# Kernel optimization log

Hardware: AMD Instinct MI355X
Metric: run time of the kernel (lower is better)

## Reference

```python
import jax, jax.numpy as jnp
import numpy as np

B, S, D = 4, 2048, 1024
EXPAND = 2
D_INNER = EXPAND * D          # 2048
D_CONV = 4
N_EXPERTS = 8
TOP_K = 2
ROUTER_HIDDEN = 128


def setup_inputs() -> dict:
    key = jax.random.key(0)
    ks = jax.random.split(key, 8)
    s = lambda fan_in: 1.0 / np.sqrt(fan_in)
    hidden_states = jax.random.normal(ks[0], (B, S, D), dtype=jnp.float32)
    # stacked per-expert SimpleSSM params (torch Linear weight layout: [out, in])
    in_proj_w = jax.random.uniform(ks[1], (N_EXPERTS, 2 * D_INNER, D), minval=-s(D), maxval=s(D), dtype=jnp.float32)
    conv_w = jax.random.uniform(ks[2], (N_EXPERTS, D_INNER, 1, D_CONV), minval=-s(D_CONV), maxval=s(D_CONV), dtype=jnp.float32)
    conv_b = jax.random.uniform(ks[3], (N_EXPERTS, D_INNER), minval=-s(D_CONV), maxval=s(D_CONV), dtype=jnp.float32)
    out_proj_w = jax.random.uniform(ks[4], (N_EXPERTS, D, D_INNER), minval=-s(D_INNER), maxval=s(D_INNER), dtype=jnp.float32)
    # router: Linear(D,128,bias=False) -> SiLU -> Linear(128,E,bias=False)
    router_w1 = jax.random.uniform(ks[5], (ROUTER_HIDDEN, D), minval=-s(D), maxval=s(D), dtype=jnp.float32)
    router_w2 = jax.random.uniform(ks[6], (N_EXPERTS, ROUTER_HIDDEN), minval=-s(ROUTER_HIDDEN), maxval=s(ROUTER_HIDDEN), dtype=jnp.float32)
    return {
        "hidden_states": hidden_states,
        "in_proj_w": in_proj_w,
        "conv_w": conv_w,
        "conv_b": conv_b,
        "out_proj_w": out_proj_w,
        "router_w1": router_w1,
        "router_w2": router_w2,
    }


def _simple_ssm(h, in_w, cw, cb, out_w):
    # h: [B,S,D]; in_w: [2*Di, D]; cw: [Di,1,4]; cb: [Di]; out_w: [D, Di]
    zx = jnp.einsum('bsd,ed->bse', h, in_w)           # [B,S,2*Di]
    z, x = jnp.split(zx, 2, axis=-1)                   # each [B,S,Di]
    xc = jnp.transpose(x, (0, 2, 1))                   # [B,Di,S]
    # torch Conv1d(padding=3, k=4) then truncate to S == causal pad (3,0) valid conv
    xc = jax.lax.conv_general_dilated(
        xc, cw, window_strides=(1,), padding=((D_CONV - 1, 0),),
        feature_group_count=D_INNER,
        dimension_numbers=('NCH', 'OIH', 'NCH'))
    xc = xc + cb[None, :, None]
    x = jnp.transpose(xc, (0, 2, 1))                   # [B,S,Di]
    x = jax.nn.silu(x) * jax.nn.silu(z)
    return jnp.einsum('bse,de->bsd', x, out_w)         # [B,S,D]


def _forward(hidden_states, in_proj_w, conv_w, conv_b, out_proj_w, router_w1, router_w2):
    # --- routing ---
    rh = jax.nn.silu(jnp.einsum('bsd,hd->bsh', hidden_states, router_w1))
    logits = jnp.einsum('bsh,eh->bse', rh, router_w2)          # [B,S,E]
    probs = jax.nn.softmax(logits, axis=-1)
    rw, sel = jax.lax.top_k(probs, TOP_K)                      # [B,S,K]
    rw = rw / jnp.sum(rw, axis=-1, keepdims=True)
    # combined per-token per-expert weight: sum_k 1[sel==e] * rw_k -> [B,S,E]
    comb = jnp.sum(jax.nn.one_hot(sel, N_EXPERTS, dtype=rw.dtype) * rw[..., None], axis=2)
    # --- each expert processes the FULL sequence ---
    expert_outs = jax.vmap(_simple_ssm, in_axes=(None, 0, 0, 0, 0))(
        hidden_states, in_proj_w, conv_w, conv_b, out_proj_w)  # [E,B,S,D]
    return jnp.einsum('ebsd,bse->bsd', expert_outs, comb)


def reference(hidden_states, in_proj_w, conv_w, conv_b, out_proj_w, router_w1, router_w2):
    return _forward(hidden_states, in_proj_w, conv_w, conv_b, out_proj_w, router_w1, router_w2)
```

## Files before the change

kernel.cpp:

```cpp
#include <hip/hip_runtime.h>
#include <hip/hip_bf16.h>
#include <stdint.h>

#define SLEN   2048
#define DMODEL 1024
#define DINNER 2048
#define NEXPERT 8
#define NTOK   8192

typedef __bf16  b8   __attribute__((ext_vector_type(8)));
typedef float   f4   __attribute__((ext_vector_type(4)));
typedef unsigned short u16x8 __attribute__((ext_vector_type(8)));

#define GLOAD16(gp, lp) __builtin_amdgcn_global_load_lds( \
    (const __attribute__((address_space(1))) uint32_t*)(gp), \
    (__attribute__((address_space(3))) uint32_t*)(lp), 16, 0, 0)

__device__ __forceinline__ unsigned short f2b(float f) {
  __hip_bfloat16 h = __float2bfloat16(f);
  return __builtin_bit_cast(unsigned short, h);
}
__device__ __forceinline__ float b2f(unsigned short u) {
  uint32_t x = ((uint32_t)u) << 16;
  return __builtin_bit_cast(float, x);
}
__device__ __forceinline__ float silu_f(float v) { return v / (1.0f + __expf(-v)); }

__global__ __launch_bounds__(256) void cast_f32_bf16(const float* __restrict__ in,
                                                     unsigned short* __restrict__ out, int n4) {
  int i = blockIdx.x * 256 + threadIdx.x;
  int stride = gridDim.x * 256;
  for (; i < n4; i += stride) {
    float4 v = ((const float4*)in)[i];
    ushort4 o;
    o.x = f2b(v.x); o.y = f2b(v.y); o.z = f2b(v.z); o.w = f2b(v.w);
    ((ushort4*)out)[i] = o;
  }
}

__global__ __launch_bounds__(256) void transpose_w1(const float* __restrict__ in,
                                                    float* __restrict__ out) {
  int idx = blockIdx.x * 256 + threadIdx.x;
  int k = idx >> 7, hd = idx & 127;
  out[idx] = in[hd * 1024 + k];
}

__global__ __launch_bounds__(256) void router_kernel(const float* __restrict__ h,
                                                     const float* __restrict__ w1T,
                                                     const float* __restrict__ w2,
                                                     float* __restrict__ comb) {
  __shared__ float hs[8 * 1024];
  __shared__ float red[2 * 8 * 128];
  __shared__ float lg[8 * 8];
  int tid = threadIdx.x;
  int t0 = blockIdx.x * 8;

  const float4* src = (const float4*)(h + (size_t)t0 * 1024);
  float4* dst = (float4*)hs;
#pragma unroll
  for (int i = 0; i < 8; ++i) dst[tid + i * 256] = src[tid + i * 256];
  __syncthreads();

  int hd = tid & 127, half = tid >> 7;
  float acc[8] = {0.f,0.f,0.f,0.f,0.f,0.f,0.f,0.f};
  int kbeg = half * 512;
  for (int k = kbeg; k < kbeg + 512; ++k) {
    float w = w1T[k * 128 + hd];
#pragma unroll
    for (int tok = 0; tok < 8; ++tok) acc[tok] += w * hs[tok * 1024 + k];
  }
#pragma unroll
  for (int tok = 0; tok < 8; ++tok) red[(half * 8 + tok) * 128 + hd] = acc[tok];
  __syncthreads();
  if (half == 0) {
#pragma unroll
    for (int tok = 0; tok < 8; ++tok) {
      float v = red[tok * 128 + hd] + red[(8 + tok) * 128 + hd];
      red[tok * 128 + hd] = silu_f(v);
    }
  }
  __syncthreads();
  if (tid < 64) {
    int e = tid & 7, tok = tid >> 3;
    float a = 0.f;
    for (int k = 0; k < 128; ++k) a += red[tok * 128 + k] * w2[e * 128 + k];
    lg[tok * 8 + e] = a;
  }
  __syncthreads();
  if (tid < 8) {
    int tok = tid;
    float* l = lg + tok * 8;
    int i0 = 0; float m0 = l[0];
    for (int e = 1; e < 8; ++e) if (l[e] > m0) { m0 = l[e]; i0 = e; }
    int i1 = -1; float m1 = -1e30f;
    for (int e = 0; e < 8; ++e) if (e != i0 && l[e] > m1) { m1 = l[e]; i1 = e; }
    float p1 = __expf(m1 - m0);
    float inv = 1.0f / (1.0f + p1);
    float* c = comb + (size_t)(t0 + tok) * 8;
#pragma unroll
    for (int e = 0; e < 8; ++e) c[e] = 0.f;
    c[i0] = inv; c[i1] = p1 * inv;
  }
}

__global__ __launch_bounds__(256) void gemm1_kernel(const unsigned short* __restrict__ A,
                                                    const unsigned short* __restrict__ BT,
                                                    unsigned short* __restrict__ C) {
  constexpr int BK = 32, K = 1024, LDA = 1024, LDB = 1024, LDC = 4096, NT = 32;
  __shared__ unsigned short As[128 * BK];
  __shared__ unsigned short Bs[128 * BK];

  int nwg = gridDim.x;
  int orig = blockIdx.x;
  int chunk = nwg >> 3;
  int logical = (orig & 7) * chunk + (orig >> 3);
  int m0 = (logical / NT) * 128, n0 = (logical % NT) * 128;

  int tid = threadIdx.x, lane = tid & 63, wid = tid >> 6;
  int wm = wid >> 1, wn = wid & 1;

  int sofs = wid * 2048 + lane * 16;
  int row0 = sofs >> 6, colel0 = (sofs & 63) >> 1;
  int sofs1 = sofs + 1024;
  int row1 = sofs1 >> 6, colel1 = (sofs1 & 63) >> 1;

  f4 zero4 = {0.f, 0.f, 0.f, 0.f};
  f4 acc[4][4];
#pragma unroll
  for (int i = 0; i < 4; ++i)
#pragma unroll
    for (int j = 0; j < 4; ++j) acc[i][j] = zero4;

  for (int k0 = 0; k0 < K; k0 += BK) {
    __syncthreads();
    GLOAD16(A  + (size_t)(m0 + row0) * LDA + k0 + colel0, (char*)As + wid * 2048);
    GLOAD16(A  + (size_t)(m0 + row1) * LDA + k0 + colel1, (char*)As + wid * 2048 + 1024);
    GLOAD16(BT + (size_t)(n0 + row0) * LDB + k0 + colel0, (char*)Bs + wid * 2048);
    GLOAD16(BT + (size_t)(n0 + row1) * LDB + k0 + colel1, (char*)Bs + wid * 2048 + 1024);
    __syncthreads();

    b8 af[4], bf[4];
#pragma unroll
    for (int mf = 0; mf < 4; ++mf) {
      int r = wm * 64 + mf * 16 + (lane & 15);
      af[mf] = __builtin_bit_cast(b8, *(const u16x8*)(As + r * BK + ((lane >> 4) << 3)));
    }
#pragma unroll
    for (int nf = 0; nf < 4; ++nf) {
      int r = wn * 64 + nf * 16 + (lane & 15);
      bf[nf] = __builtin_bit_cast(b8, *(const u16x8*)(Bs + r * BK + ((lane >> 4) << 3)));
    }
#pragma unroll
    for (int mf = 0; mf < 4; ++mf)
#pragma unroll
      for (int nf = 0; nf < 4; ++nf)
        acc[mf][nf] = __builtin_amdgcn_mfma_f32_16x16x32_bf16(af[mf], bf[nf], acc[mf][nf], 0, 0, 0);
  }

#pragma unroll
  for (int mf = 0; mf < 4; ++mf)
#pragma unroll
    for (int r = 0; r < 4; ++r) {
      int row = m0 + wm * 64 + mf * 16 + ((lane >> 4) << 2) + r;
#pragma unroll
      for (int nf = 0; nf < 4; ++nf) {
        int col = n0 + wn * 64 + nf * 16 + (lane & 15);
        C[(size_t)row * LDC + col] = f2b(acc[mf][nf][r]);
      }
    }
}

__global__ __launch_bounds__(256) void conv_kernel(const unsigned short* __restrict__ zx,
                                                   const float* __restrict__ conv_w,
                                                   const float* __restrict__ conv_b,
                                                   const float* __restrict__ comb,
                                                   unsigned short* __restrict__ xact,
                                                   int e) {
  int t = blockIdx.x;
  int s = t & (SLEN - 1);
  int c0 = threadIdx.x * 8;
  float cv = comb[(size_t)t * 8 + e];

  u16x8 z = *(const u16x8*)(zx + (size_t)t * 4096 + c0);
  u16x8 x[4];
  u16x8 zv = {0,0,0,0,0,0,0,0};
#pragma unroll
  for (int j = 0; j < 4; ++j) {
    int srow = s - 3 + j;
    x[j] = (srow >= 0) ? *(const u16x8*)(zx + (size_t)(t - 3 + j) * 4096 + 2048 + c0) : zv;
  }
  const float4* cw = (const float4*)(conv_w + ((size_t)e * 2048 + c0) * 4);
  const float4* cb4 = (const float4*)(conv_b + (size_t)e * 2048 + c0);
  float4 blo = cb4[0], bhi = cb4[1];
  float bias[8] = {blo.x, blo.y, blo.z, blo.w, bhi.x, bhi.y, bhi.z, bhi.w};

  u16x8 res;
#pragma unroll
  for (int i = 0; i < 8; ++i) {
    float4 w = cw[i];
    float xc = bias[i] + w.x * b2f(x[0][i]) + w.y * b2f(x[1][i])
                       + w.z * b2f(x[2][i]) + w.w * b2f(x[3][i]);
    float o = silu_f(xc) * silu_f(b2f(z[i])) * cv;
    res[i] = f2b(o);
  }
  *(u16x8*)(xact + (size_t)t * (NEXPERT * DINNER) + (size_t)e * DINNER + c0) = res;
}

__global__ __launch_bounds__(256) void gemm2_kernel(const unsigned short* __restrict__ A,
                                                    const unsigned short* __restrict__ BTa,
                                                    float* __restrict__ C) {
  constexpr int BK = 32, LDA = 16384, LDB = 2048, LDC = 1024, NT = 8;
  __shared__ unsigned short As[128 * BK];
  __shared__ unsigned short Bs[128 * BK];

  int nwg = gridDim.x;
  int orig = blockIdx.x;
  int chunk = nwg >> 3;
  int logical = (orig & 7) * chunk + (orig >> 3);
  int m0 = (logical / NT) * 128, n0 = (logical % NT) * 128;

  int tid = threadIdx.x, lane = tid & 63, wid = tid >> 6;
  int wm = wid >> 1, wn = wid & 1;

  int sofs = wid * 2048 + lane * 16;
  int row0 = sofs >> 6, colel0 = (sofs & 63) >> 1;
  int sofs1 = sofs + 1024;
  int row1 = sofs1 >> 6, colel1 = (sofs1 & 63) >> 1;

  f4 zero4 = {0.f, 0.f, 0.f, 0.f};
  f4 acc[4][4];
#pragma unroll
  for (int i = 0; i < 4; ++i)
#pragma unroll
    for (int j = 0; j < 4; ++j) acc[i][j] = zero4;

  for (int e = 0; e < NEXPERT; ++e) {
    const unsigned short* BT = BTa + (size_t)e * 1024 * 2048;
    int kbase = e * 2048;
    for (int k0 = 0; k0 < 2048; k0 += BK) {
      __syncthreads();
      GLOAD16(A  + (size_t)(m0 + row0) * LDA + kbase + k0 + colel0, (char*)As + wid * 2048);
      GLOAD16(A  + (size_t)(m0 + row1) * LDA + kbase + k0 + colel1, (char*)As + wid * 2048 + 1024);
      GLOAD16(BT + (size_t)(n0 + row0) * LDB + k0 + colel0,         (char*)Bs + wid * 2048);
      GLOAD16(BT + (size_t)(n0 + row1) * LDB + k0 + colel1,         (char*)Bs + wid * 2048 + 1024);
      __syncthreads();

      b8 af[4], bf[4];
#pragma unroll
      for (int mf = 0; mf < 4; ++mf) {
        int r = wm * 64 + mf * 16 + (lane & 15);
        af[mf] = __builtin_bit_cast(b8, *(const u16x8*)(As + r * BK + ((lane >> 4) << 3)));
      }
#pragma unroll
      for (int nf = 0; nf < 4; ++nf) {
        int r = wn * 64 + nf * 16 + (lane & 15);
        bf[nf] = __builtin_bit_cast(b8, *(const u16x8*)(Bs + r * BK + ((lane >> 4) << 3)));
      }
#pragma unroll
      for (int mf = 0; mf < 4; ++mf)
#pragma unroll
        for (int nf = 0; nf < 4; ++nf)
          acc[mf][nf] = __builtin_amdgcn_mfma_f32_16x16x32_bf16(af[mf], bf[nf], acc[mf][nf], 0, 0, 0);
    }
  }

#pragma unroll
  for (int mf = 0; mf < 4; ++mf)
#pragma unroll
    for (int r = 0; r < 4; ++r) {
      int row = m0 + wm * 64 + mf * 16 + ((lane >> 4) << 2) + r;
#pragma unroll
      for (int nf = 0; nf < 4; ++nf) {
        int col = n0 + wn * 64 + nf * 16 + (lane & 15);
        C[(size_t)row * LDC + col] = acc[mf][nf][r];
      }
    }
}

extern "C" void kernel_launch(void* const* d_in, const int* in_sizes, int n_in,
                              void* d_out, int out_size, void* d_ws, size_t ws_size,
                              hipStream_t stream) {
  const float* h      = (const float*)d_in[0];
  const float* in_w   = (const float*)d_in[1];
  const float* conv_w = (const float*)d_in[2];
  const float* conv_b = (const float*)d_in[3];
  const float* out_w  = (const float*)d_in[4];
  const float* r_w1   = (const float*)d_in[5];
  const float* r_w2   = (const float*)d_in[6];
  float* out = (float*)d_out;

  char* ws = (char*)d_ws;
  unsigned short* h_bf    = (unsigned short*)(ws);
  unsigned short* inw_bf  = (unsigned short*)(ws + 16777216);
  unsigned short* outw_bf = (unsigned short*)(ws + 83886080);
  float*          w1T     = (float*)(ws + 117440512);
  float*          comb    = (float*)(ws + 117964800);
  unsigned short* zx_e    = (unsigned short*)(ws + 118226944);
  unsigned short* xact    = (unsigned short*)(ws + 185335808);
  if (ws_size < 453771264ull) return;

  cast_f32_bf16<<<2048, 256, 0, stream>>>(h,     h_bf,    8388608 / 4);
  cast_f32_bf16<<<2048, 256, 0, stream>>>(in_w,  inw_bf,  33554432 / 4);
  cast_f32_bf16<<<2048, 256, 0, stream>>>(out_w, outw_bf, 16777216 / 4);
  transpose_w1<<<512, 256, 0, stream>>>(r_w1, w1T);
  router_kernel<<<1024, 256, 0, stream>>>(h, w1T, r_w2, comb);

  for (int e = 0; e < NEXPERT; ++e) {
    gemm1_kernel<<<2048, 256, 0, stream>>>(h_bf, inw_bf + (size_t)e * 4096 * 1024, zx_e);
    conv_kernel<<<8192, 256, 0, stream>>>(zx_e, conv_w, conv_b, comb, xact, e);
  }
  gemm2_kernel<<<512, 256, 0, stream>>>(xact, outw_bf, out);
}
```

Before: 1.860 ms.

## Replace GEMMs with 256-tile double-buffered, swizzled, pipelined MFMA kernel

Both GEMMs now use one templated 512-thread kernel with 256xBN tiles and BK=64. It double-buffers shared memory through async global-to-LDS loads, waits on explicit vmcnt counts, and XOR-swizzles LDS rows to avoid bank conflicts. Each k-step is split into quarter phases that interleave loads with MFMA bursts, and MFMA priority is raised during those bursts. This targets the sync-heavy, low-reuse 128x128 BK=32 loop, at the cost of more LDS and registers, lower occupancy, and hand-tuned wait counts that are fragile.

```diff
diff --git a/kernel.cpp b/kernel.cpp
--- a/kernel.cpp
+++ b/kernel.cpp
@@ -15,6 +15,14 @@
 #define GLOAD16(gp, lp) __builtin_amdgcn_global_load_lds( \
     (const __attribute__((address_space(1))) uint32_t*)(gp), \
     (__attribute__((address_space(3))) uint32_t*)(lp), 16, 0, 0)
+
+#define VM4()   asm volatile("s_waitcnt vmcnt(4)" ::: "memory")
+#define VM3()   asm volatile("s_waitcnt vmcnt(3)" ::: "memory")
+#define VM0()   asm volatile("s_waitcnt vmcnt(0)" ::: "memory")
+#define LGKM0() asm volatile("s_waitcnt lgkmcnt(0)" ::: "memory")
+#define FENCE() asm volatile("" ::: "memory")
+#define SB()    __builtin_amdgcn_s_barrier()
+#define SCHED0() __builtin_amdgcn_sched_barrier(0)
 
 __device__ __forceinline__ unsigned short f2b(float f) {
   __hip_bfloat16 h = __float2bfloat16(f);
@@ -103,71 +111,139 @@
   }
 }
 
-__global__ __launch_bounds__(256) void gemm1_kernel(const unsigned short* __restrict__ A,
-                                                    const unsigned short* __restrict__ BT,
-                                                    unsigned short* __restrict__ C) {
-  constexpr int BK = 32, K = 1024, LDA = 1024, LDB = 1024, LDC = 4096, NT = 32;
-  __shared__ unsigned short As[128 * BK];
-  __shared__ unsigned short Bs[128 * BK];
-
-  int nwg = gridDim.x;
-  int orig = blockIdx.x;
-  int chunk = nwg >> 3;
-  int logical = (orig & 7) * chunk + (orig >> 3);
-  int m0 = (logical / NT) * 128, n0 = (logical % NT) * 128;
-
-  int tid = threadIdx.x, lane = tid & 63, wid = tid >> 6;
-  int wm = wid >> 1, wn = wid & 1;
-
-  int sofs = wid * 2048 + lane * 16;
-  int row0 = sofs >> 6, colel0 = (sofs & 63) >> 1;
-  int sofs1 = sofs + 1024;
-  int row1 = sofs1 >> 6, colel1 = (sofs1 & 63) >> 1;
-
-  f4 zero4 = {0.f, 0.f, 0.f, 0.f};
-  f4 acc[4][4];
-#pragma unroll
-  for (int i = 0; i < 4; ++i)
-#pragma unroll
-    for (int j = 0; j < 4; ++j) acc[i][j] = zero4;
-
-  for (int k0 = 0; k0 < K; k0 += BK) {
-    __syncthreads();
-    GLOAD16(A  + (size_t)(m0 + row0) * LDA + k0 + colel0, (char*)As + wid * 2048);
-    GLOAD16(A  + (size_t)(m0 + row1) * LDA + k0 + colel1, (char*)As + wid * 2048 + 1024);
-    GLOAD16(BT + (size_t)(n0 + row0) * LDB + k0 + colel0, (char*)Bs + wid * 2048);
-    GLOAD16(BT + (size_t)(n0 + row1) * LDB + k0 + colel1, (char*)Bs + wid * 2048 + 1024);
-    __syncthreads();
-
-    b8 af[4], bf[4];
-#pragma unroll
-    for (int mf = 0; mf < 4; ++mf) {
-      int r = wm * 64 + mf * 16 + (lane & 15);
-      af[mf] = __builtin_bit_cast(b8, *(const u16x8*)(As + r * BK + ((lane >> 4) << 3)));
-    }
-#pragma unroll
-    for (int nf = 0; nf < 4; ++nf) {
-      int r = wn * 64 + nf * 16 + (lane & 15);
-      bf[nf] = __builtin_bit_cast(b8, *(const u16x8*)(Bs + r * BK + ((lane >> 4) << 3)));
-    }
-#pragma unroll
-    for (int mf = 0; mf < 4; ++mf)
-#pragma unroll
-      for (int nf = 0; nf < 4; ++nf)
-        acc[mf][nf] = __builtin_amdgcn_mfma_f32_16x16x32_bf16(af[mf], bf[nf], acc[mf][nf], 0, 0, 0);
-  }
-
-#pragma unroll
-  for (int mf = 0; mf < 4; ++mf)
-#pragma unroll
-    for (int r = 0; r < 4; ++r) {
-      int row = m0 + wm * 64 + mf * 16 + ((lane >> 4) << 2) + r;
-#pragma unroll
-      for (int nf = 0; nf < 4; ++nf) {
-        int col = n0 + wn * 64 + nf * 16 + (lane & 15);
-        C[(size_t)row * LDC + col] = f2b(acc[mf][nf][r]);
+template<int BN, int K, int LDA, int LDB, int LDC, int NTN, bool OUTBF, bool BSPLIT>
+__global__ __launch_bounds__(512, 2) void gemm256(const unsigned short* __restrict__ A,
+                                                  const unsigned short* __restrict__ Bm,
+                                                  void* __restrict__ Cv) {
+  constexpr int NT = K / 64;
+  constexpr int NH = BN / 128;
+  constexpr int BH = (BN / 2) * 128;
+  constexpr int BW = BH / 8;
+  __shared__ char smem[65536 + 4 * BH];
+  char* Asm = smem;
+  char* Bsm = smem + 65536;
+
+  const int nwg = gridDim.x;
+  const int chunk = nwg >> 3;
+  const int wg = ((int)blockIdx.x & 7) * chunk + ((int)blockIdx.x >> 3);
+  const int mt = wg / NTN, nt = wg % NTN;
+  const int m0 = mt * 256, n0 = nt * BN;
+
+  const int tid = threadIdx.x, lane = tid & 63, wid = tid >> 6;
+  const int wm = wid >> 2, wn = wid & 3;
+  const int l15 = lane & 15, hi16 = (lane >> 4) << 4, swx = (lane & 7) << 4;
+
+  const int l3 = lane >> 3;
+  const int scol = ((lane & 7) ^ l3) << 3;
+  const int lrA0 = wid * 16 + l3, lrA1 = lrA0 + 8;
+  const int rA0 = ((lrA0 >> 6) << 7) + (lrA0 & 63);
+  const int rA1 = ((lrA1 >> 6) << 7) + (lrA1 & 63);
+  int rB0_ = 0, rB1_ = 0;
+  if (BN == 256) {
+    int lr0 = wid * 16 + l3, lr1 = lr0 + 8;
+    rB0_ = ((lr0 >> 5) << 6) + (lr0 & 31);
+    rB1_ = ((lr1 >> 5) << 6) + (lr1 & 31);
+  } else {
+    int lr0 = wid * 8 + l3;
+    rB0_ = ((lr0 >> 4) << 5) + (lr0 & 15);
+  }
+  const int rB0 = rB0_, rB1 = rB1_;
+
+#define STAGE_A(p, h, k0) do {                                            \
+    char* _d = Asm + (p) * 32768 + (h) * 16384 + wid * 2048;              \
+    GLOAD16(A + (size_t)(m0 + rA0 + (h) * 64) * LDA + (k0) + scol, _d);   \
+    GLOAD16(A + (size_t)(m0 + rA1 + (h) * 64) * LDA + (k0) + scol, _d + 1024); \
+  } while (0)
+
+#define STAGE_B(p, h, k0) do {                                            \
+    const unsigned short* _B = Bm; int _kk = (k0);                        \
+    if (BSPLIT) { _B = Bm + (size_t)((k0) >> 11) * 2097152; _kk = (k0) & 2047; } \
+    char* _d = Bsm + (p) * (2 * BH) + (h) * BH + wid * BW;                \
+    if (BN == 256) {                                                      \
+      GLOAD16(_B + (size_t)(n0 + rB0 + (h) * (BN/8)) * LDB + _kk + scol, _d);        \
+      GLOAD16(_B + (size_t)(n0 + rB1 + (h) * (BN/8)) * LDB + _kk + scol, _d + 1024); \
+    } else {                                                              \
+      GLOAD16(_B + (size_t)(n0 + rB0 + (h) * (BN/8)) * LDB + _kk + scol, _d);        \
+    }                                                                     \
+  } while (0)
+
+  b8 af[4][2];
+  b8 bfr[NH][2];
+  f4 acc[8][2 * NH];
+#pragma unroll
+  for (int i = 0; i < 8; ++i)
+#pragma unroll
+    for (int j = 0; j < 2 * NH; ++j) { f4 z = {0.f,0.f,0.f,0.f}; acc[i][j] = z; }
+
+#define READ_A(mh, cur) do {                                              \
+    const char* _b = Asm + (cur) * 32768 + (mh) * 16384 + (wm * 64 + l15) * 128; \
+    _Pragma("unroll") for (int mfl = 0; mfl < 4; ++mfl)                   \
+    _Pragma("unroll") for (int ks = 0; ks < 2; ++ks)                      \
+      af[mfl][ks] = *(const b8*)(_b + mfl * 2048 + ((ks * 64 + hi16) ^ swx)); \
+  } while (0)
+
+#define READ_B(nh, cur) do {                                              \
+    const char* _b = Bsm + (cur) * (2 * BH) + (nh) * BH + (wn * (BN/8) + l15) * 128; \
+    _Pragma("unroll") for (int nfl = 0; nfl < NH; ++nfl)                  \
+    _Pragma("unroll") for (int ks = 0; ks < 2; ++ks)                      \
+      bfr[nfl][ks] = *(const b8*)(_b + nfl * 2048 + ((ks * 64 + hi16) ^ swx)); \
+  } while (0)
+
+#define MFMA_Q(mh, nh) do {                                               \
+    _Pragma("unroll") for (int mfl = 0; mfl < 4; ++mfl)                   \
+    _Pragma("unroll") for (int nfl = 0; nfl < NH; ++nfl)                  \
+    _Pragma("unroll") for (int ks = 0; ks < 2; ++ks)                      \
+      acc[(mh)*4+mfl][(nh)*NH+nfl] = __builtin_amdgcn_mfma_f32_16x16x32_bf16( \
+          af[mfl][ks], bfr[nfl][ks], acc[(mh)*4+mfl][(nh)*NH+nfl], 0, 0, 0);  \
+  } while (0)
+
+  STAGE_A(0, 0, 0);  STAGE_B(0, 1, 0);  STAGE_A(0, 1, 0);  STAGE_B(0, 0, 0);
+  STAGE_A(1, 0, 64); STAGE_B(1, 1, 64);
+
+  for (int t = 0; t < NT; ++t) {
+    const int cur = t & 1, nxt = cur ^ 1;
+    const int k1 = (t + 1) * 64, k2 = (t + 2) * 64;
+    const bool s1 = (t + 1) < NT, s2 = (t + 2) < NT;
+    if (t == NT - 1) { VM0(); } else if (BN == 256) { VM4(); } else { VM3(); }
+    SB(); FENCE();
+    READ_A(0, cur); READ_B(0, cur);
+    if (s1) STAGE_A(nxt, 1, k1);
+    LGKM0(); SCHED0();
+    __builtin_amdgcn_s_setprio(1); MFMA_Q(0, 0); __builtin_amdgcn_s_setprio(0);
+    SB(); FENCE();
+    READ_B(1, cur);
+    if (s1) STAGE_B(nxt, 0, k1);
+    LGKM0(); SCHED0();
+    __builtin_amdgcn_s_setprio(1); MFMA_Q(0, 1); __builtin_amdgcn_s_setprio(0);
+    SB(); FENCE();
+    READ_A(1, cur);
+    if (s2) STAGE_A(cur, 0, k2);
+    LGKM0(); SCHED0();
+    __builtin_amdgcn_s_setprio(1); MFMA_Q(1, 1); __builtin_amdgcn_s_setprio(0);
+    SB(); FENCE();
+    READ_B(0, cur);
+    if (s2) STAGE_B(cur, 1, k2);
+    LGKM0(); SCHED0();
+    __builtin_amdgcn_s_setprio(1); MFMA_Q(1, 0); __builtin_amdgcn_s_setprio(0);
+  }
+
+  const int r0 = m0 + wm * 128 + ((lane >> 4) << 2);
+  const int c0 = n0 + wn * (BN / 4) + l15;
+#pragma unroll
+  for (int mf = 0; mf < 8; ++mf)
+#pragma unroll
+    for (int nf = 0; nf < 2 * NH; ++nf)
+#pragma unroll
+      for (int r = 0; r < 4; ++r) {
+        size_t off = (size_t)(r0 + mf * 16 + r) * LDC + (c0 + nf * 16);
+        if (OUTBF) ((unsigned short*)Cv)[off] = f2b(acc[mf][nf][r]);
+        else       ((float*)Cv)[off] = acc[mf][nf][r];
       }
-    }
+#undef STAGE_A
+#undef STAGE_B
+#undef READ_A
+#undef READ_B
+#undef MFMA_Q
 }
 
 __global__ __launch_bounds__(256) void conv_kernel(const unsigned short* __restrict__ zx,
@@ -204,77 +280,6 @@
     res[i] = f2b(o);
   }
   *(u16x8*)(xact + (size_t)t * (NEXPERT * DINNER) + (size_t)e * DINNER + c0) = res;
-}
-
-__global__ __launch_bounds__(256) void gemm2_kernel(const unsigned short* __restrict__ A,
-                                                    const unsigned short* __restrict__ BTa,
-                                                    float* __restrict__ C) {
-  constexpr int BK = 32, LDA = 16384, LDB = 2048, LDC = 1024, NT = 8;
-  __shared__ unsigned short As[128 * BK];
-  __shared__ unsigned short Bs[128 * BK];
-
-  int nwg = gridDim.x;
-  int orig = blockIdx.x;
-  int chunk = nwg >> 3;
-  int logical = (orig & 7) * chunk + (orig >> 3);
-  int m0 = (logical / NT) * 128, n0 = (logical % NT) * 128;
-
-  int tid = threadIdx.x, lane = tid & 63, wid = tid >> 6;
-  int wm = wid >> 1, wn = wid & 1;
-
-  int sofs = wid * 2048 + lane * 16;
-  int row0 = sofs >> 6, colel0 = (sofs & 63) >> 1;
-  int sofs1 = sofs + 1024;
-  int row1 = sofs1 >> 6, colel1 = (sofs1 & 63) >> 1;
-
-  f4 zero4 = {0.f, 0.f, 0.f, 0.f};
-  f4 acc[4][4];
-#pragma unroll
-  for (int i = 0; i < 4; ++i)
-#pragma unroll
-    for (int j = 0; j < 4; ++j) acc[i][j] = zero4;
-
-  for (int e = 0; e < NEXPERT; ++e) {
-    const unsigned short* BT = BTa + (size_t)e * 1024 * 2048;
-    int kbase = e * 2048;
-    for (int k0 = 0; k0 < 2048; k0 += BK) {
-      __syncthreads();
-      GLOAD16(A  + (size_t)(m0 + row0) * LDA + kbase + k0 + colel0, (char*)As + wid * 2048);
-      GLOAD16(A  + (size_t)(m0 + row1) * LDA + kbase + k0 + colel1, (char*)As + wid * 2048 + 1024);
-      GLOAD16(BT + (size_t)(n0 + row0) * LDB + k0 + colel0,         (char*)Bs + wid * 2048);
-      GLOAD16(BT + (size_t)(n0 + row1) * LDB + k0 + colel1,         (char*)Bs + wid * 2048 + 1024);
-      __syncthreads();
-
-      b8 af[4], bf[4];
-#pragma unroll
-      for (int mf = 0; mf < 4; ++mf) {
-        int r = wm * 64 + mf * 16 + (lane & 15);
-        af[mf] = __builtin_bit_cast(b8, *(const u16x8*)(As + r * BK + ((lane >> 4) << 3)));
-      }
-#pragma unroll
-      for (int nf = 0; nf < 4; ++nf) {
-        int r = wn * 64 + nf * 16 + (lane & 15);
-        bf[nf] = __builtin_bit_cast(b8, *(const u16x8*)(Bs + r * BK + ((lane >> 4) << 3)));
-      }
-#pragma unroll
-      for (int mf = 0; mf < 4; ++mf)
-#pragma unroll
-        for (int nf = 0; nf < 4; ++nf)
-          acc[mf][nf] = __builtin_amdgcn_mfma_f32_16x16x32_bf16(af[mf], bf[nf], acc[mf][nf], 0, 0, 0);
-    }
-  }
-
-#pragma unroll
-  for (int mf = 0; mf < 4; ++mf)
-#pragma unroll
-    for (int r = 0; r < 4; ++r) {
-      int row = m0 + wm * 64 + mf * 16 + ((lane >> 4) << 2) + r;
-#pragma unroll
-      for (int nf = 0; nf < 4; ++nf) {
-        int col = n0 + wn * 64 + nf * 16 + (lane & 15);
-        C[(size_t)row * LDC + col] = acc[mf][nf][r];
-      }
-    }
 }
 
 extern "C" void kernel_launch(void* const* d_in, const int* in_sizes, int n_in,
@@ -306,8 +311,10 @@
   router_kernel<<<1024, 256, 0, stream>>>(h, w1T, r_w2, comb);
 
   for (int e = 0; e < NEXPERT; ++e) {
-    gemm1_kernel<<<2048, 256, 0, stream>>>(h_bf, inw_bf + (size_t)e * 4096 * 1024, zx_e);
+    gemm256<256, 1024, 1024, 1024, 4096, 16, true, false>
+        <<<512, 512, 0, stream>>>(h_bf, inw_bf + (size_t)e * 4096 * 1024, zx_e);
     conv_kernel<<<8192, 256, 0, stream>>>(zx_e, conv_w, conv_b, comb, xact, e);
   }
-  gemm2_kernel<<<512, 256, 0, stream>>>(xact, outw_bf, out);
-}
+  gemm256<128, 16384, 16384, 2048, 1024, 8, false, true>
+      <<<256, 512, 0, stream>>>(xact, outw_bf, out);
+}
```

New measurement: 1.562 ms. -16.0%, faster.
